# Kernel optimization log

Measured on AMD Instinct MI355X. Metric: run time of the kernel, lower is better.

## Reference

```python
import jax, jax.numpy as jnp
import numpy as np

B, DX, DY, H = 512, 128, 128, 512


def setup_inputs() -> dict:
    key = jax.random.key(0)
    ks = jax.random.split(key, 6)
    x = jax.random.normal(ks[0], (B, DX), dtype=jnp.float32)
    y = jax.random.normal(ks[1], (B, DY), dtype=jnp.float32)
    # MLP params: Linear(DX+DY, H) -> ReLU -> Linear(H, H) -> ReLU -> Linear(H, 1)
    W1 = jax.random.normal(ks[2], (DX + DY, H), dtype=jnp.float32) / np.sqrt(DX + DY)
    b1 = jnp.zeros((H,), dtype=jnp.float32)
    W2 = jax.random.normal(ks[3], (H, H), dtype=jnp.float32) / np.sqrt(H)
    b2 = jnp.zeros((H,), dtype=jnp.float32)
    W3 = jax.random.normal(ks[4], (H, 1), dtype=jnp.float32) / np.sqrt(H)
    b3 = jnp.zeros((1,), dtype=jnp.float32)
    return {"x": x, "y": y, "W1": W1, "b1": b1, "W2": W2, "b2": b2, "W3": W3, "b3": b3}


def reference(x, y, W1, b1, W2, b2, W3, b3):
    # scores[i, j] = MLP(concat(x_i, y_j)).
    # The first linear layer is separable in x and y: split W1 and broadcast-add,
    # avoiding materializing the [B^2, DX+DY] concat tensor.
    dx = x.shape[-1]
    W1x, W1y = W1[:dx], W1[dx:]
    hx = x @ W1x                      # [B, H]
    hy = y @ W1y                      # [B, H]
    h1 = jax.nn.relu(hx[:, None, :] + hy[None, :, :] + b1)   # [B, B, H]
    h2 = jax.nn.relu(jnp.einsum('ijh,hk->ijk', h1, W2) + b2)  # [B, B, H]
    scores = jnp.einsum('ijh,ho->ijo', h2, W3) + b3           # [B, B, 1]
    return scores[..., 0]             # [B, B]
```

## Files before the change

### kernel.cpp

```cpp
#include <hip/hip_runtime.h>
#include <hip/hip_bf16.h>

typedef __bf16 bf16x8 __attribute__((ext_vector_type(8)));
typedef float  f32x4  __attribute__((ext_vector_type(4)));
typedef float  f32x16 __attribute__((ext_vector_type(16)));

#define B_  512
#define DX_ 128
#define H_  512

__global__ __launch_bounds__(256) void prep_kernel(
    const float* __restrict__ x, const float* __restrict__ y,
    const float* __restrict__ W1, const float* __restrict__ W2,
    const float* __restrict__ b1,
    __bf16* __restrict__ PW2, float* __restrict__ hx, float* __restrict__ hyb)
{
    int blk = blockIdx.x;
    int tid = threadIdx.x;
    if (blk < 128) {
        int u   = blk * 256 + tid;
        int ks2 = u >> 10;
        int rem = u & 1023;
        int nt  = rem >> 6;
        int l   = rem & 63;
        int k   = ks2 * 16 + ((l >> 5) << 3);
        int col = nt * 32 + (l & 31);
        const float* p = W2 + k * H_ + col;
        bf16x8 v;
        #pragma unroll
        for (int j = 0; j < 8; ++j) v[j] = (__bf16)p[j * H_];
        *(bf16x8*)(PW2 + u * 8) = v;
        return;
    }
    int b    = blk - 128;
    int task = b >> 5;
    int rem  = b & 31;
    int bm   = rem >> 2, bn = rem & 3;
    const float* A  = task ? y : x;
    const float* Wp = W1 + task * DX_ * H_;
    float* outp = task ? hyb : hx;
    int w = tid >> 6, lane = tid & 63;

    f32x4 acc[4][2] = {};
    #pragma unroll
    for (int ks = 0; ks < 4; ++ks) {
        int k0 = ks * 32 + ((lane >> 4) << 3);
        bf16x8 af[4];
        #pragma unroll
        for (int mt = 0; mt < 4; ++mt) {
            int row = bm * 64 + mt * 16 + (lane & 15);
            const float* pa = A + row * DX_ + k0;
            f32x4 q0 = *(const f32x4*)pa;
            f32x4 q1 = *(const f32x4*)(pa + 4);
            #pragma unroll
            for (int j = 0; j < 4; ++j) {
                af[mt][j]     = (__bf16)q0[j];
                af[mt][j + 4] = (__bf16)q1[j];
            }
        }
        #pragma unroll
        for (int nt = 0; nt < 2; ++nt) {
            int col = bn * 128 + (w * 2 + nt) * 16 + (lane & 15);
            const float* pb = Wp + k0 * H_ + col;
            bf16x8 bv;
            #pragma unroll
            for (int j = 0; j < 8; ++j) bv[j] = (__bf16)pb[j * H_];
            #pragma unroll
            for (int mt = 0; mt < 4; ++mt)
                acc[mt][nt] = __builtin_amdgcn_mfma_f32_16x16x32_bf16(af[mt], bv, acc[mt][nt], 0, 0, 0);
        }
    }
    #pragma unroll
    for (int nt = 0; nt < 2; ++nt) {
        int col = bn * 128 + (w * 2 + nt) * 16 + (lane & 15);
        float badd = task ? b1[col] : 0.f;
        #pragma unroll
        for (int mt = 0; mt < 4; ++mt) {
            #pragma unroll
            for (int r = 0; r < 4; ++r) {
                int row = bm * 64 + mt * 16 + ((lane >> 4) << 2) + r;
                outp[row * H_ + col] = acc[mt][nt][r] + badd;
            }
        }
    }
}

__global__ __launch_bounds__(512, 2) void critic_kernel(
    const float* __restrict__ hx, const float* __restrict__ hyb,
    const __bf16* __restrict__ PW2,
    const float* __restrict__ b2, const float* __restrict__ W3,
    const float* __restrict__ b3, float* __restrict__ out)
{
    __shared__ float hx_s[16 * 516];
    __shared__ float hy_s[8 * 516];
    __shared__ __align__(16) char h1_s[3 * 8192];
    __shared__ float sc_s[128];

    int tid = threadIdx.x;
    int lane = tid & 63, wid = tid >> 6;
    int mw = wid >> 2, nw = wid & 3;
    int bj = blockIdx.x, bi = blockIdx.y;

    for (int idx = tid; idx < 16 * 128; idx += 512) {
        int r = idx >> 7, c4 = (idx & 127) << 2;
        *(f32x4*)&hx_s[r * 516 + c4] = *(const f32x4*)&hx[(bi * 16 + r) * H_ + c4];
    }
    for (int idx = tid; idx < 8 * 128; idx += 512) {
        int r = idx >> 7, c4 = (idx & 127) << 2;
        *(f32x4*)&hy_s[r * 516 + c4] = *(const f32x4*)&hyb[(bj * 8 + r) * H_ + c4];
    }
    if (tid < 128) sc_s[tid] = 0.f;

    int grow = tid >> 2, q = tid & 3;
    const float* px = &hx_s[(grow >> 3) * 516 + q * 8];
    const float* py = &hy_s[(grow & 7) * 516 + q * 8];
    const int woff = grow * 64 + ((q ^ ((grow >> 1) & 3)) << 4);

    int aoff[2][2];
    #pragma unroll
    for (int t = 0; t < 2; ++t)
        #pragma unroll
        for (int mt = 0; mt < 2; ++mt) {
            int row  = mw * 64 + mt * 32 + (lane & 31);
            int slot = (t * 2 + (lane >> 5)) ^ ((row >> 1) & 3);
            aoff[t][mt] = row * 64 + (slot << 4);
        }

    f32x16 acc[2][4] = {};

    auto GEN = [&](int g) {
        const f32x4 a0 = *(const f32x4*)(px + g * 32);
        const f32x4 a1 = *(const f32x4*)(px + g * 32 + 4);
        const f32x4 c0 = *(const f32x4*)(py + g * 32);
        const f32x4 c1 = *(const f32x4*)(py + g * 32 + 4);
        f32x4 s0 = a0 + c0, s1 = a1 + c1;
        bf16x8 hv;
        #pragma unroll
        for (int j = 0; j < 4; ++j) {
            hv[j]     = (__bf16)fmaxf(s0[j], 0.f);
            hv[j + 4] = (__bf16)fmaxf(s1[j], 0.f);
        }
        *(bf16x8*)(h1_s + (g % 3) * 8192 + woff) = hv;
    };

    auto STEP = [&](int ks) {
        const char* base = h1_s + (ks % 3) * 8192;
        bf16x8 a00 = *(const bf16x8*)(base + aoff[0][0]);
        bf16x8 a01 = *(const bf16x8*)(base + aoff[0][1]);
        bf16x8 a10 = *(const bf16x8*)(base + aoff[1][0]);
        bf16x8 a11 = *(const bf16x8*)(base + aoff[1][1]);
        const __bf16* pb = PW2 + ((ks * 2) * 16 + nw * 4) * 512 + lane * 8;
        #pragma unroll
        for (int t = 0; t < 2; ++t) {
            #pragma unroll
            for (int nt = 0; nt < 4; ++nt) {
                bf16x8 bv = *(const bf16x8*)(pb + t * 8192 + nt * 512);
                acc[0][nt] = __builtin_amdgcn_mfma_f32_32x32x16_bf16(t ? a10 : a00, bv, acc[0][nt], 0, 0, 0);
                acc[1][nt] = __builtin_amdgcn_mfma_f32_32x32x16_bf16(t ? a11 : a01, bv, acc[1][nt], 0, 0, 0);
            }
        }
    };

    __syncthreads();
    GEN(0);
    GEN(1);
    __syncthreads();

    #pragma unroll
    for (int ks = 0; ks < 16; ++ks) {
        if (mw == 0) {
            STEP(ks);
            if (ks < 14) GEN(ks + 2);
        } else {
            if (ks < 14) GEN(ks + 2);
            STEP(ks);
        }
        if (ks < 15) __syncthreads();
    }

    float b2v[4], w3v[4];
    #pragma unroll
    for (int nt = 0; nt < 4; ++nt) {
        int col = nw * 128 + nt * 32 + (lane & 31);
        b2v[nt] = b2[col];
        w3v[nt] = W3[col];
    }
    #pragma unroll
    for (int mt = 0; mt < 2; ++mt) {
        #pragma unroll
        for (int r = 0; r < 16; ++r) {
            float s = 0.f;
            #pragma unroll
            for (int nt = 0; nt < 4; ++nt) {
                float h2 = fmaxf(acc[mt][nt][r] + b2v[nt], 0.f);
                s += h2 * w3v[nt];
            }
            s += __shfl_xor(s, 1);
            s += __shfl_xor(s, 2);
            s += __shfl_xor(s, 4);
            s += __shfl_xor(s, 8);
            s += __shfl_xor(s, 16);
            if ((lane & 31) == 0) {
                int prow = mw * 64 + mt * 32 + ((r & 3) + 8 * (r >> 2)) + ((lane >> 5) << 2);
                atomicAdd(&sc_s[prow], s);
            }
        }
    }
    __syncthreads();
    if (tid < 128) {
        int i = bi * 16 + (tid >> 3);
        int j = bj * 8 + (tid & 7);
        out[i * B_ + j] = sc_s[tid] + b3[0];
    }
}

extern "C" void kernel_launch(void* const* d_in, const int* in_sizes, int n_in,
                              void* d_out, int out_size, void* d_ws, size_t ws_size,
                              hipStream_t stream)
{
    const float* x  = (const float*)d_in[0];
    const float* y  = (const float*)d_in[1];
    const float* W1 = (const float*)d_in[2];
    const float* b1 = (const float*)d_in[3];
    const float* W2 = (const float*)d_in[4];
    const float* b2 = (const float*)d_in[5];
    const float* W3 = (const float*)d_in[6];
    const float* b3 = (const float*)d_in[7];
    float* out = (float*)d_out;

    char* ws = (char*)d_ws;
    float*  hx  = (float*)(ws);
    float*  hyb = (float*)(ws + 1048576);
    __bf16* PW2 = (__bf16*)(ws + 2097152);

    hipLaunchKernelGGL(prep_kernel, dim3(192), dim3(256), 0, stream,
                       x, y, W1, W2, b1, PW2, hx, hyb);
    hipLaunchKernelGGL(critic_kernel, dim3(64, 32), dim3(512), 0, stream,
                       hx, hyb, PW2, b2, W3, b3, out);
}
```

Before: 261.4 us.

## Drop shared-memory staging; each wave builds h1 in registers and atomically accumulates scores

```diff
diff --git a/kernel.cpp b/kernel.cpp
--- a/kernel.cpp
+++ b/kernel.cpp
@@ -85,132 +85,101 @@
     }
 }
 
-__global__ __launch_bounds__(512, 2) void critic_kernel(
+__global__ __launch_bounds__(256, 2) void critic_kernel(
     const float* __restrict__ hx, const float* __restrict__ hyb,
     const __bf16* __restrict__ PW2,
     const float* __restrict__ b2, const float* __restrict__ W3,
     const float* __restrict__ b3, float* __restrict__ out)
 {
-    __shared__ float hx_s[16 * 516];
-    __shared__ float hy_s[8 * 516];
-    __shared__ __align__(16) char h1_s[3 * 8192];
-    __shared__ float sc_s[128];
-
-    int tid = threadIdx.x;
-    int lane = tid & 63, wid = tid >> 6;
-    int mw = wid >> 2, nw = wid & 3;
-    int bj = blockIdx.x, bi = blockIdx.y;
-
-    for (int idx = tid; idx < 16 * 128; idx += 512) {
-        int r = idx >> 7, c4 = (idx & 127) << 2;
-        *(f32x4*)&hx_s[r * 516 + c4] = *(const f32x4*)&hx[(bi * 16 + r) * H_ + c4];
-    }
-    for (int idx = tid; idx < 8 * 128; idx += 512) {
-        int r = idx >> 7, c4 = (idx & 127) << 2;
-        *(f32x4*)&hy_s[r * 516 + c4] = *(const f32x4*)&hyb[(bj * 8 + r) * H_ + c4];
-    }
-    if (tid < 128) sc_s[tid] = 0.f;
-
-    int grow = tid >> 2, q = tid & 3;
-    const float* px = &hx_s[(grow >> 3) * 516 + q * 8];
-    const float* py = &hy_s[(grow & 7) * 516 + q * 8];
-    const int woff = grow * 64 + ((q ^ ((grow >> 1) & 3)) << 4);
-
-    int aoff[2][2];
-    #pragma unroll
-    for (int t = 0; t < 2; ++t)
-        #pragma unroll
-        for (int mt = 0; mt < 2; ++mt) {
-            int row  = mw * 64 + mt * 32 + (lane & 31);
-            int slot = (t * 2 + (lane >> 5)) ^ ((row >> 1) & 3);
-            aoff[t][mt] = row * 64 + (slot << 4);
-        }
+    int tid  = threadIdx.x;
+    int lane = tid & 63;
+    int W    = blockIdx.x * 4 + (tid >> 6);
+    int c    = W & 3;
+    int t    = W >> 2;
+    int ib   = t >> 6, jb = t & 63;
+
+    int o   = lane >> 5;
+    int r31 = lane & 31;
+
+    const float* hx0 = hx  + (ib * 8 + (r31 >> 3)) * H_ + o * 8;
+    const float* hx1 = hx0 + 4 * H_;
+    const float* hyp = hyb + (jb * 8 + (lane & 7)) * H_ + o * 8;
+    const __bf16* pb = PW2 + (c * 4) * 512 + lane * 8;
 
     f32x16 acc[2][4] = {};
 
-    auto GEN = [&](int g) {
-        const f32x4 a0 = *(const f32x4*)(px + g * 32);
-        const f32x4 a1 = *(const f32x4*)(px + g * 32 + 4);
-        const f32x4 c0 = *(const f32x4*)(py + g * 32);
-        const f32x4 c1 = *(const f32x4*)(py + g * 32 + 4);
-        f32x4 s0 = a0 + c0, s1 = a1 + c1;
-        bf16x8 hv;
-        #pragma unroll
-        for (int j = 0; j < 4; ++j) {
-            hv[j]     = (__bf16)fmaxf(s0[j], 0.f);
-            hv[j + 4] = (__bf16)fmaxf(s1[j], 0.f);
-        }
-        *(bf16x8*)(h1_s + (g % 3) * 8192 + woff) = hv;
+    f32x4  xa[2][2][2];
+    f32x4  ya[2][2];
+    bf16x8 bv[2][4];
+
+    auto LOADA = [&](int s, int buf) {
+        xa[buf][0][0] = *(const f32x4*)(hx0 + s * 16);
+        xa[buf][0][1] = *(const f32x4*)(hx0 + s * 16 + 4);
+        xa[buf][1][0] = *(const f32x4*)(hx1 + s * 16);
+        xa[buf][1][1] = *(const f32x4*)(hx1 + s * 16 + 4);
+        ya[buf][0]    = *(const f32x4*)(hyp + s * 16);
+        ya[buf][1]    = *(const f32x4*)(hyp + s * 16 + 4);
     };
-
-    auto STEP = [&](int ks) {
-        const char* base = h1_s + (ks % 3) * 8192;
-        bf16x8 a00 = *(const bf16x8*)(base + aoff[0][0]);
-        bf16x8 a01 = *(const bf16x8*)(base + aoff[0][1]);
-        bf16x8 a10 = *(const bf16x8*)(base + aoff[1][0]);
-        bf16x8 a11 = *(const bf16x8*)(base + aoff[1][1]);
-        const __bf16* pb = PW2 + ((ks * 2) * 16 + nw * 4) * 512 + lane * 8;
-        #pragma unroll
-        for (int t = 0; t < 2; ++t) {
-            #pragma unroll
-            for (int nt = 0; nt < 4; ++nt) {
-                bf16x8 bv = *(const bf16x8*)(pb + t * 8192 + nt * 512);
-                acc[0][nt] = __builtin_amdgcn_mfma_f32_32x32x16_bf16(t ? a10 : a00, bv, acc[0][nt], 0, 0, 0);
-                acc[1][nt] = __builtin_amdgcn_mfma_f32_32x32x16_bf16(t ? a11 : a01, bv, acc[1][nt], 0, 0, 0);
-            }
-        }
+    auto LOADB = [&](int s, int buf) {
+        const __bf16* p = pb + s * 8192;
+        #pragma unroll
+        for (int nt = 0; nt < 4; ++nt) bv[buf][nt] = *(const bf16x8*)(p + nt * 512);
     };
-
-    __syncthreads();
-    GEN(0);
-    GEN(1);
-    __syncthreads();
-
-    #pragma unroll
-    for (int ks = 0; ks < 16; ++ks) {
-        if (mw == 0) {
-            STEP(ks);
-            if (ks < 14) GEN(ks + 2);
-        } else {
-            if (ks < 14) GEN(ks + 2);
-            STEP(ks);
-        }
-        if (ks < 15) __syncthreads();
+    auto COMPUTE = [&](int buf) {
+        bf16x8 a[2];
+        #pragma unroll
+        for (int mt = 0; mt < 2; ++mt)
+            #pragma unroll
+            for (int j = 0; j < 4; ++j) {
+                a[mt][j]     = (__bf16)fmaxf(xa[buf][mt][0][j] + ya[buf][0][j], 0.f);
+                a[mt][j + 4] = (__bf16)fmaxf(xa[buf][mt][1][j] + ya[buf][1][j], 0.f);
+            }
+        __builtin_amdgcn_s_setprio(1);
+        #pragma unroll
+        for (int nt = 0; nt < 4; ++nt) {
+            acc[0][nt] = __builtin_amdgcn_mfma_f32_32x32x16_bf16(a[0], bv[buf][nt], acc[0][nt], 0, 0, 0);
+            acc[1][nt] = __builtin_amdgcn_mfma_f32_32x32x16_bf16(a[1], bv[buf][nt], acc[1][nt], 0, 0, 0);
+        }
+        __builtin_amdgcn_s_setprio(0);
+    };
+
+    LOADA(0, 0); LOADB(0, 0);
+    for (int sp = 0; sp < 16; ++sp) {
+        int s0 = sp * 2;
+        LOADA(s0 + 1, 1); LOADB(s0 + 1, 1);
+        COMPUTE(0);
+        if (sp < 15) { LOADA(s0 + 2, 0); LOADB(s0 + 2, 0); }
+        COMPUTE(1);
     }
 
     float b2v[4], w3v[4];
     #pragma unroll
     for (int nt = 0; nt < 4; ++nt) {
-        int col = nw * 128 + nt * 32 + (lane & 31);
+        int col = c * 128 + nt * 32 + r31;
         b2v[nt] = b2[col];
         w3v[nt] = W3[col];
     }
+    float bq = 0.25f * b3[0];
     #pragma unroll
     for (int mt = 0; mt < 2; ++mt) {
         #pragma unroll
-        for (int r = 0; r < 16; ++r) {
+        for (int rg = 0; rg < 16; ++rg) {
             float s = 0.f;
             #pragma unroll
-            for (int nt = 0; nt < 4; ++nt) {
-                float h2 = fmaxf(acc[mt][nt][r] + b2v[nt], 0.f);
-                s += h2 * w3v[nt];
-            }
+            for (int nt = 0; nt < 4; ++nt)
+                s += fmaxf(acc[mt][nt][rg] + b2v[nt], 0.f) * w3v[nt];
             s += __shfl_xor(s, 1);
             s += __shfl_xor(s, 2);
             s += __shfl_xor(s, 4);
             s += __shfl_xor(s, 8);
             s += __shfl_xor(s, 16);
-            if ((lane & 31) == 0) {
-                int prow = mw * 64 + mt * 32 + ((r & 3) + 8 * (r >> 2)) + ((lane >> 5) << 2);
-                atomicAdd(&sc_s[prow], s);
-            }
-        }
-    }
-    __syncthreads();
-    if (tid < 128) {
-        int i = bi * 16 + (tid >> 3);
-        int j = bj * 8 + (tid & 7);
-        out[i * B_ + j] = sc_s[tid] + b3[0];
+            if (r31 == 0) {
+                int pl = mt * 32 + (rg & 3) + 8 * (rg >> 2) + (o << 2);
+                int i  = ib * 8 + (pl >> 3);
+                int j  = jb * 8 + (pl & 7);
+                atomicAdd(&out[i * B_ + j], s + bq);
+            }
+        }
     }
 }
 
@@ -233,8 +202,9 @@
     float*  hyb = (float*)(ws + 1048576);
     __bf16* PW2 = (__bf16*)(ws + 2097152);
 
+    hipMemsetAsync(d_out, 0, (size_t)out_size * sizeof(float), stream);
     hipLaunchKernelGGL(prep_kernel, dim3(192), dim3(256), 0, stream,
                        x, y, W1, W2, b1, PW2, hx, hyb);
-    hipLaunchKernelGGL(critic_kernel, dim3(64, 32), dim3(512), 0, stream,
+    hipLaunchKernelGGL(critic_kernel, dim3(4096), dim3(256), 0, stream,
                        hx, hyb, PW2, b2, W3, b3, out);
 }
```

After: 314.2 us. +20.2%, slower.
